# Performance work log

Measured on AMD Instinct MI355X. Metric: run time of the kernel, lower is better.

The kernel has to match this reference:

```python
import jax, jax.numpy as jnp
import numpy as np

IN_FEATURES = 4096
OUT_FEATURES = 16384


def setup_inputs() -> dict:
    key = jax.random.key(0)
    k_x, k_w, k_s, k_b = jax.random.split(key, 4)
    x = jax.random.normal(k_x, (2, 2048, IN_FEATURES), dtype=jnp.float32)
    # quantized weights take integer values in [-7, 7] like the triton kernel output
    weight_quantized = jax.random.randint(k_w, (OUT_FEATURES, IN_FEATURES), -7, 8, dtype=jnp.int32)
    # per-output-row scales (abs_max/7 style, strictly positive)
    weight_scale = jax.random.uniform(k_s, (OUT_FEATURES,), dtype=jnp.float32, minval=0.001, maxval=0.1)
    bias = jax.random.normal(k_b, (OUT_FEATURES,), dtype=jnp.float32) * 0.02
    return {"x": x, "weight_quantized": weight_quantized, "weight_scale": weight_scale, "bias": bias}


def reference(x, weight_quantized, weight_scale, bias):
    # dequantize: fp32 weight [out, in] = int8 weight * per-row scale
    weight = weight_quantized.astype(jnp.float32) * weight_scale[:, None]
    # F.linear: x @ weight.T + bias  -> [B, S, out]
    out = jnp.einsum('bsi,oi->bso', x, weight) + bias
    return out
```

## Files before the change

kernel.cpp:

```cpp
#include <hip/hip_runtime.h>
#include <stdint.h>

#define M_TOT 4096
#define K_DIM 4096
#define N_DIM 16384

typedef __attribute__((ext_vector_type(4))) int i32x4;

__device__ __forceinline__ int pack4(float a, float b, float c, float d, float inv) {
  int q0 = __float2int_rn(a * inv) & 255;
  int q1 = __float2int_rn(b * inv) & 255;
  int q2 = __float2int_rn(c * inv) & 255;
  int q3 = __float2int_rn(d * inv);
  return q0 | (q1 << 8) | (q2 << 16) | (q3 << 24);
}

__global__ __launch_bounds__(256)
void quant_x_k(const float* __restrict__ x, int4* __restrict__ xq,
               float* __restrict__ rowScale) {
  const int row = blockIdx.x;
  const int tid = threadIdx.x;
  const float* xr = x + (size_t)row * K_DIM + tid * 16;
  float4 v[4];
  float m = 0.f;
#pragma unroll
  for (int i = 0; i < 4; ++i) {
    v[i] = *(const float4*)(xr + i * 4);
    m = fmaxf(m, fmaxf(fmaxf(fabsf(v[i].x), fabsf(v[i].y)),
                       fmaxf(fabsf(v[i].z), fabsf(v[i].w))));
  }
#pragma unroll
  for (int off = 32; off > 0; off >>= 1)
    m = fmaxf(m, __shfl_xor(m, off));
  __shared__ float wmx[4];
  if ((tid & 63) == 0) wmx[tid >> 6] = m;
  __syncthreads();
  m = fmaxf(fmaxf(wmx[0], wmx[1]), fmaxf(wmx[2], wmx[3]));
  m = fmaxf(m, 1e-20f);
  if (tid == 0) rowScale[row] = m / 127.f;
  const float inv = 127.f / m;
  int4 o;
  o.x = pack4(v[0].x, v[0].y, v[0].z, v[0].w, inv);
  o.y = pack4(v[1].x, v[1].y, v[1].z, v[1].w, inv);
  o.z = pack4(v[2].x, v[2].y, v[2].z, v[2].w, inv);
  o.w = pack4(v[3].x, v[3].y, v[3].z, v[3].w, inv);
  xq[((size_t)row * K_DIM >> 4) + tid] = o;
}

__global__ void cvt_w_k(const int4* __restrict__ src, int4* __restrict__ dst, int n16) {
  int stride = gridDim.x * blockDim.x;
  for (int i = blockIdx.x * blockDim.x + threadIdx.x; i < n16; i += stride) {
    int4 o;
#pragma unroll
    for (int j = 0; j < 4; ++j) {
      int4 v = src[i * 4 + j];
      int p = (v.x & 255) | ((v.y & 255) << 8) | ((v.z & 255) << 16) | (v.w << 24);
      (&o.x)[j] = p;
    }
    dst[i] = o;
  }
}

__device__ __forceinline__ void gload16(const void* g, void* l) {
  __builtin_amdgcn_global_load_lds(
      (__attribute__((address_space(1))) void*)(g),
      (__attribute__((address_space(3))) void*)(l),
      16, 0, 0);
}

#define SWZ(o) ((o) ^ ((((o) >> 7) & 7) << 4))

#define MFMA_I8(a, b, c) __builtin_amdgcn_mfma_i32_16x16x64_i8(a, b, c, 0, 0, 0)

__global__ __launch_bounds__(512, 2)
void gemm_i8(const char* __restrict__ A, const char* __restrict__ W,
             const float* __restrict__ rowScale, const float* __restrict__ scale,
             const float* __restrict__ bias, float* __restrict__ C) {
  __shared__ __align__(16) char lds[131072];
  char* lbase = lds;

  const int tid  = threadIdx.x;
  const int lane = tid & 63;
  const int wave = tid >> 6;
  const int wm   = wave >> 2;
  const int wn   = wave & 3;
  const int r    = lane & 15;
  const int kq16 = (lane >> 4) << 4;

  const int nwg  = gridDim.x;
  const int bid  = blockIdx.x;
  const int wgid = (bid & 7) * (nwg >> 3) + (bid >> 3);
  const int tm   = wgid >> 6;
  const int tn   = wgid & 63;
  const int row0 = tm * 256;
  const int col0 = tn * 256;

  int s_row0, s_col0, s_row1, s_col1;
  {
    int l0 = SWZ(tid * 16);
    int l1 = SWZ(8192 + tid * 16);
    s_row0 = l0 >> 6; s_col0 = l0 & 63;
    s_row1 = l1 >> 6; s_col1 = l1 & 63;
  }

  auto STAGE = [&](const char* G, int rb, int kb, int blkB) {
    gload16(G + (size_t)(rb + s_row0) * K_DIM + kb + s_col0,
            lbase + blkB + (wave << 10));
    gload16(G + (size_t)(rb + s_row1) * K_DIM + kb + s_col1,
            lbase + blkB + 8192 + (wave << 10));
  };

  i32x4 acc[8][4];
#pragma unroll
  for (int i = 0; i < 8; ++i)
#pragma unroll
    for (int j = 0; j < 4; ++j)
      acc[i][j] = (i32x4){0, 0, 0, 0};

  STAGE(A, row0, 0,   0);
  STAGE(W, col0, 0,   32768);
  STAGE(A, row0, 64,  16384);
  STAGE(W, col0, 64,  49152);
  STAGE(A, row0, 128, 65536);
  STAGE(W, col0, 128, 98304);
  asm volatile("s_waitcnt vmcnt(4)" ::: "memory");
  __builtin_amdgcn_s_barrier();

  i32x4 a[4], b[4];

  for (int t = 0; t < 32; ++t) {
    const int cur  = t & 1;
    const int curB = cur << 16;
    const int nxtB = (cur ^ 1) << 16;
    const int kb1  = ((t + 1 < 32) ? t + 1 : 31) * 128;
    const int kb2  = ((t + 2 < 32) ? t + 2 : 31) * 128;

#pragma unroll
    for (int q = 0; q < 4; ++q)
      a[q] = *(const i32x4*)(lbase + curB + SWZ(((wm * 128 + q * 16 + r) << 6) + kq16));
#pragma unroll
    for (int q = 0; q < 4; ++q)
      b[q] = *(const i32x4*)(lbase + curB + 32768 + SWZ(((wn * 64 + q * 16 + r) << 6) + kq16));
    STAGE(A, row0, kb1 + 64, nxtB + 16384);
    __builtin_amdgcn_s_setprio(1);
#pragma unroll
    for (int mi = 0; mi < 4; ++mi)
#pragma unroll
      for (int ni = 0; ni < 4; ++ni)
        acc[mi][ni] = MFMA_I8(a[mi], b[ni], acc[mi][ni]);
    __builtin_amdgcn_s_setprio(0);
    __builtin_amdgcn_s_barrier();

#pragma unroll
    for (int q = 0; q < 4; ++q)
      a[q] = *(const i32x4*)(lbase + curB + SWZ(((wm * 128 + (4 + q) * 16 + r) << 6) + kq16));
    STAGE(W, col0, kb1 + 64, nxtB + 49152);
    __builtin_amdgcn_s_setprio(1);
#pragma unroll
    for (int mi = 0; mi < 4; ++mi)
#pragma unroll
      for (int ni = 0; ni < 4; ++ni)
        acc[4 + mi][ni] = MFMA_I8(a[mi], b[ni], acc[4 + mi][ni]);
    __builtin_amdgcn_s_setprio(0);
    __builtin_amdgcn_s_barrier();

#pragma unroll
    for (int q = 0; q < 4; ++q)
      a[q] = *(const i32x4*)(lbase + curB + 16384 + SWZ(((wm * 128 + q * 16 + r) << 6) + kq16));
#pragma unroll
    for (int q = 0; q < 4; ++q)
      b[q] = *(const i32x4*)(lbase + curB + 49152 + SWZ(((wn * 64 + q * 16 + r) << 6) + kq16));
    STAGE(A, row0, kb2, curB);
    __builtin_amdgcn_s_setprio(1);
#pragma unroll
    for (int mi = 0; mi < 4; ++mi)
#pragma unroll
      for (int ni = 0; ni < 4; ++ni)
        acc[mi][ni] = MFMA_I8(a[mi], b[ni], acc[mi][ni]);
    __builtin_amdgcn_s_setprio(0);
    __builtin_amdgcn_s_barrier();

#pragma unroll
    for (int q = 0; q < 4; ++q)
      a[q] = *(const i32x4*)(lbase + curB + 16384 + SWZ(((wm * 128 + (4 + q) * 16 + r) << 6) + kq16));
    STAGE(W, col0, kb2, curB + 32768);
    __builtin_amdgcn_s_setprio(1);
#pragma unroll
    for (int mi = 0; mi < 4; ++mi)
#pragma unroll
      for (int ni = 0; ni < 4; ++ni)
        acc[4 + mi][ni] = MFMA_I8(a[mi], b[ni], acc[4 + mi][ni]);
    __builtin_amdgcn_s_setprio(0);
    asm volatile("s_waitcnt vmcnt(4)" ::: "memory");
    __builtin_amdgcn_s_barrier();
  }

  asm volatile("s_waitcnt vmcnt(0)" ::: "memory");

  const int kq = kq16 >> 4;
  float rsv[8][4];
#pragma unroll
  for (int mi = 0; mi < 8; ++mi) {
    const int rowb = row0 + wm * 128 + mi * 16 + kq * 4;
#pragma unroll
    for (int q = 0; q < 4; ++q)
      rsv[mi][q] = rowScale[rowb + q];
  }
#pragma unroll
  for (int ni = 0; ni < 4; ++ni) {
    const int col = col0 + wn * 64 + ni * 16 + r;
    const float sc = scale[col];
    const float bv = bias[col];
#pragma unroll
    for (int mi = 0; mi < 8; ++mi) {
      const int rowb = row0 + wm * 128 + mi * 16 + kq * 4;
#pragma unroll
      for (int q = 0; q < 4; ++q)
        C[(size_t)(rowb + q) * N_DIM + col] =
            (float)acc[mi][ni][q] * (rsv[mi][q] * sc) + bv;
    }
  }
}

extern "C" void kernel_launch(void* const* d_in, const int* in_sizes, int n_in,
                              void* d_out, int out_size, void* d_ws, size_t ws_size,
                              hipStream_t stream) {
  const float* x      = (const float*)d_in[0];
  const int*   wq     = (const int*)d_in[1];
  const float* wscale = (const float*)d_in[2];
  const float* wbias  = (const float*)d_in[3];
  float* out = (float*)d_out;

  const size_t xq_bytes = (size_t)M_TOT * K_DIM;
  const size_t wq_bytes = (size_t)N_DIM * K_DIM;
  const size_t rs_bytes = (size_t)M_TOT * 4;
  if (ws_size < xq_bytes + wq_bytes + rs_bytes) return;

  char*  xq8 = (char*)d_ws;
  char*  wq8 = (char*)d_ws + xq_bytes;
  float* rs  = (float*)((char*)d_ws + xq_bytes + wq_bytes);

  quant_x_k<<<M_TOT, 256, 0, stream>>>(x, (int4*)xq8, rs);
  cvt_w_k<<<2048, 256, 0, stream>>>((const int4*)wq, (int4*)wq8,
                                    (N_DIM * K_DIM) / 16);

  const int grid = (M_TOT / 256) * (N_DIM / 256);
  gemm_i8<<<grid, 512, 0, stream>>>(xq8, wq8, rs, wscale, wbias, out);
}
```

Measured before the change: 385.4 us.

## Restructure int8 GEMM staging into 128-wide K tiles with one barrier per step

```diff
diff --git a/kernel.cpp b/kernel.cpp
--- a/kernel.cpp
+++ b/kernel.cpp
@@ -95,20 +95,16 @@
   const int row0 = tm * 256;
   const int col0 = tn * 256;
 
-  int s_row0, s_col0, s_row1, s_col1;
-  {
-    int l0 = SWZ(tid * 16);
-    int l1 = SWZ(8192 + tid * 16);
-    s_row0 = l0 >> 6; s_col0 = l0 & 63;
-    s_row1 = l1 >> 6; s_col1 = l1 & 63;
-  }
-
-  auto STAGE = [&](const char* G, int rb, int kb, int blkB) {
-    gload16(G + (size_t)(rb + s_row0) * K_DIM + kb + s_col0,
-            lbase + blkB + (wave << 10));
-    gload16(G + (size_t)(rb + s_row1) * K_DIM + kb + s_col1,
-            lbase + blkB + 8192 + (wave << 10));
-  };
+  size_t tOff[4];
+#pragma unroll
+  for (int j = 0; j < 4; ++j) {
+    int l = SWZ(j * 8192 + tid * 16);
+    tOff[j] = (size_t)(l >> 7) * K_DIM + (l & 127);
+  }
+  const int tid16 = tid * 16;
+
+  const char* Arow = A + (size_t)row0 * K_DIM;
+  const char* Wrow = W + (size_t)col0 * K_DIM;
 
   i32x4 acc[8][4];
 #pragma unroll
@@ -117,31 +113,35 @@
     for (int j = 0; j < 4; ++j)
       acc[i][j] = (i32x4){0, 0, 0, 0};
 
-  STAGE(A, row0, 0,   0);
-  STAGE(W, col0, 0,   32768);
-  STAGE(A, row0, 64,  16384);
-  STAGE(W, col0, 64,  49152);
-  STAGE(A, row0, 128, 65536);
-  STAGE(W, col0, 128, 98304);
-  asm volatile("s_waitcnt vmcnt(4)" ::: "memory");
+#pragma unroll
+  for (int j = 0; j < 4; ++j)
+    gload16(Arow + tOff[j], lbase + j * 8192 + tid16);
+#pragma unroll
+  for (int j = 0; j < 4; ++j)
+    gload16(Wrow + tOff[j], lbase + 32768 + j * 8192 + tid16);
+  asm volatile("s_waitcnt vmcnt(0)" ::: "memory");
   __builtin_amdgcn_s_barrier();
 
   i32x4 a[4], b[4];
 
   for (int t = 0; t < 32; ++t) {
-    const int cur  = t & 1;
-    const int curB = cur << 16;
-    const int nxtB = (cur ^ 1) << 16;
+    const int curB = (t & 1) << 16;
+    const int nxtB = curB ^ 65536;
     const int kb1  = ((t + 1 < 32) ? t + 1 : 31) * 128;
-    const int kb2  = ((t + 2 < 32) ? t + 2 : 31) * 128;
-
-#pragma unroll
-    for (int q = 0; q < 4; ++q)
-      a[q] = *(const i32x4*)(lbase + curB + SWZ(((wm * 128 + q * 16 + r) << 6) + kq16));
-#pragma unroll
-    for (int q = 0; q < 4; ++q)
-      b[q] = *(const i32x4*)(lbase + curB + 32768 + SWZ(((wn * 64 + q * 16 + r) << 6) + kq16));
-    STAGE(A, row0, kb1 + 64, nxtB + 16384);
+
+#pragma unroll
+    for (int j = 0; j < 4; ++j)
+      gload16(Arow + kb1 + tOff[j], lbase + nxtB + j * 8192 + tid16);
+#pragma unroll
+    for (int j = 0; j < 4; ++j)
+      gload16(Wrow + kb1 + tOff[j], lbase + nxtB + 32768 + j * 8192 + tid16);
+
+#pragma unroll
+    for (int q = 0; q < 4; ++q)
+      a[q] = *(const i32x4*)(lbase + curB + SWZ(((wm * 128 + q * 16 + r) << 7) + kq16));
+#pragma unroll
+    for (int q = 0; q < 4; ++q)
+      b[q] = *(const i32x4*)(lbase + curB + 32768 + SWZ(((wn * 64 + q * 16 + r) << 7) + kq16));
     __builtin_amdgcn_s_setprio(1);
 #pragma unroll
     for (int mi = 0; mi < 4; ++mi)
@@ -149,53 +149,46 @@
       for (int ni = 0; ni < 4; ++ni)
         acc[mi][ni] = MFMA_I8(a[mi], b[ni], acc[mi][ni]);
     __builtin_amdgcn_s_setprio(0);
+
+#pragma unroll
+    for (int q = 0; q < 4; ++q)
+      a[q] = *(const i32x4*)(lbase + curB + SWZ(((wm * 128 + (4 + q) * 16 + r) << 7) + kq16));
+    __builtin_amdgcn_s_setprio(1);
+#pragma unroll
+    for (int mi = 0; mi < 4; ++mi)
+#pragma unroll
+      for (int ni = 0; ni < 4; ++ni)
+        acc[4 + mi][ni] = MFMA_I8(a[mi], b[ni], acc[4 + mi][ni]);
+    __builtin_amdgcn_s_setprio(0);
+
+#pragma unroll
+    for (int q = 0; q < 4; ++q)
+      a[q] = *(const i32x4*)(lbase + curB + SWZ(((wm * 128 + q * 16 + r) << 7) + 64 + kq16));
+#pragma unroll
+    for (int q = 0; q < 4; ++q)
+      b[q] = *(const i32x4*)(lbase + curB + 32768 + SWZ(((wn * 64 + q * 16 + r) << 7) + 64 + kq16));
+    __builtin_amdgcn_s_setprio(1);
+#pragma unroll
+    for (int mi = 0; mi < 4; ++mi)
+#pragma unroll
+      for (int ni = 0; ni < 4; ++ni)
+        acc[mi][ni] = MFMA_I8(a[mi], b[ni], acc[mi][ni]);
+    __builtin_amdgcn_s_setprio(0);
+
+#pragma unroll
+    for (int q = 0; q < 4; ++q)
+      a[q] = *(const i32x4*)(lbase + curB + SWZ(((wm * 128 + (4 + q) * 16 + r) << 7) + 64 + kq16));
+    __builtin_amdgcn_s_setprio(1);
+#pragma unroll
+    for (int mi = 0; mi < 4; ++mi)
+#pragma unroll
+      for (int ni = 0; ni < 4; ++ni)
+        acc[4 + mi][ni] = MFMA_I8(a[mi], b[ni], acc[4 + mi][ni]);
+    __builtin_amdgcn_s_setprio(0);
+
+    asm volatile("s_waitcnt vmcnt(0)" ::: "memory");
     __builtin_amdgcn_s_barrier();
-
-#pragma unroll
-    for (int q = 0; q < 4; ++q)
-      a[q] = *(const i32x4*)(lbase + curB + SWZ(((wm * 128 + (4 + q) * 16 + r) << 6) + kq16));
-    STAGE(W, col0, kb1 + 64, nxtB + 49152);
-    __builtin_amdgcn_s_setprio(1);
-#pragma unroll
-    for (int mi = 0; mi < 4; ++mi)
-#pragma unroll
-      for (int ni = 0; ni < 4; ++ni)
-        acc[4 + mi][ni] = MFMA_I8(a[mi], b[ni], acc[4 + mi][ni]);
-    __builtin_amdgcn_s_setprio(0);
-    __builtin_amdgcn_s_barrier();
-
-#pragma unroll
-    for (int q = 0; q < 4; ++q)
-      a[q] = *(const i32x4*)(lbase + curB + 16384 + SWZ(((wm * 128 + q * 16 + r) << 6) + kq16));
-#pragma unroll
-    for (int q = 0; q < 4; ++q)
-      b[q] = *(const i32x4*)(lbase + curB + 49152 + SWZ(((wn * 64 + q * 16 + r) << 6) + kq16));
-    STAGE(A, row0, kb2, curB);
-    __builtin_amdgcn_s_setprio(1);
-#pragma unroll
-    for (int mi = 0; mi < 4; ++mi)
-#pragma unroll
-      for (int ni = 0; ni < 4; ++ni)
-        acc[mi][ni] = MFMA_I8(a[mi], b[ni], acc[mi][ni]);
-    __builtin_amdgcn_s_setprio(0);
-    __builtin_amdgcn_s_barrier();
-
-#pragma unroll
-    for (int q = 0; q < 4; ++q)
-      a[q] = *(const i32x4*)(lbase + curB + 16384 + SWZ(((wm * 128 + (4 + q) * 16 + r) << 6) + kq16));
-    STAGE(W, col0, kb2, curB + 32768);
-    __builtin_amdgcn_s_setprio(1);
-#pragma unroll
-    for (int mi = 0; mi < 4; ++mi)
-#pragma unroll
-      for (int ni = 0; ni < 4; ++ni)
-        acc[4 + mi][ni] = MFMA_I8(a[mi], b[ni], acc[4 + mi][ni]);
-    __builtin_amdgcn_s_setprio(0);
-    asm volatile("s_waitcnt vmcnt(4)" ::: "memory");
-    __builtin_amdgcn_s_barrier();
-  }
-
-  asm volatile("s_waitcnt vmcnt(0)" ::: "memory");
+  }
 
   const int kq = kq16 >> 4;
   float rsv[8][4];
```

Result: no change. 381.7 us (-1.0%).
